# Kernel tuning notes

Measured on AMD Instinct MI355X. Metric: run time of the kernel, lower is better.

## Reference

```python
import jax, jax.numpy as jnp
import numpy as np

DIM = 768
NUM_HEADS = 12
HEAD_DIM = DIM // NUM_HEADS
SCALE = HEAD_DIM ** -0.5


def setup_inputs() -> dict:
    key = jax.random.key(0)
    k1, k2, k3, k4 = jax.random.split(key, 4)
    B, H, W = 8, 32, 32
    x = jax.random.normal(k1, (B, H, W, DIM), dtype=jnp.float32)
    s = DIM ** -0.5
    w_qkv = jax.random.normal(k2, (DIM, 3 * DIM), dtype=jnp.float32) * s
    w_proj = jax.random.normal(k3, (DIM, DIM), dtype=jnp.float32) * s
    b_proj = jax.random.normal(k4, (DIM,), dtype=jnp.float32) * 0.01
    return {"x": x, "w_qkv": w_qkv, "w_proj": w_proj, "b_proj": b_proj}


def reference(x, w_qkv, w_proj, b_proj):
    B, H, W, C = x.shape
    N = H * W
    qkv = (x.reshape(B, N, C) @ w_qkv).reshape(B, N, 3, NUM_HEADS, HEAD_DIM)
    q, k, v = jnp.moveaxis(qkv, 2, 0)  # each (B, N, h, d)
    # scores: (B, h, N, N)
    attn = jnp.einsum('bnhd,bmhd->bhnm', q * SCALE, k)
    attn = jax.nn.softmax(attn, axis=-1)
    out = jnp.einsum('bhnm,bmhd->bnhd', attn, v).reshape(B, H, W, C)
    return out @ w_proj + b_proj
```

## Files before the change

kernel.cpp:

```cpp
#include <hip/hip_runtime.h>

typedef _Float16 half_t;
typedef __attribute__((ext_vector_type(4))) _Float16 half4;
typedef __attribute__((ext_vector_type(8))) _Float16 half8;
typedef __attribute__((ext_vector_type(4))) float floatx4;

#define MFMA_F16(A,B,C)  __builtin_amdgcn_mfma_f32_16x16x32_f16(A,B,C,0,0,0)

typedef __attribute__((address_space(1))) const void gvoid_t;
typedef __attribute__((address_space(3))) void svoid_t;

__device__ __forceinline__ void async_copy16(const half_t* g, half_t* l) {
    __builtin_amdgcn_global_load_lds((gvoid_t*)g, (svoid_t*)l, 16, 0, 0);
}

__global__ __launch_bounds__(256)
void prep_kernel(const float* __restrict__ x, const float* __restrict__ w_qkv,
                 const float* __restrict__ w_proj, half_t* __restrict__ xh,
                 half_t* __restrict__ wqkvT, half_t* __restrict__ wprojT)
{
    __shared__ half_t tile[64 * 65];
    const int id = blockIdx.x, tid = threadIdx.x;
    if (id < 6144) {
        size_t e = (size_t)id * 1024 + tid * 4;
        float4 f = *(const float4*)(x + e);
        half4 h = { (half_t)f.x, (half_t)f.y, (half_t)f.z, (half_t)f.w };
        *(half4*)(xh + e) = h;
        return;
    }
    const float* src; half_t* dst; int lds, tr0, tc0;
    if (id < 6576) { int t = id - 6144; src = w_qkv; dst = wqkvT; lds = 2304;
                     tr0 = (t / 36) * 64; tc0 = (t % 36) * 64; }
    else           { int t = id - 6576; src = w_proj; dst = wprojT; lds = 768;
                     tr0 = (t / 12) * 64; tc0 = (t % 12) * 64; }
    #pragma unroll
    for (int i = 0; i < 4; i++) {
        int e = tid + i * 256, r = e >> 4, c4 = (e & 15) << 2;
        float4 f = *(const float4*)(src + (size_t)(tr0 + r) * lds + tc0 + c4);
        tile[(c4 + 0) * 65 + r] = (half_t)f.x;
        tile[(c4 + 1) * 65 + r] = (half_t)f.y;
        tile[(c4 + 2) * 65 + r] = (half_t)f.z;
        tile[(c4 + 3) * 65 + r] = (half_t)f.w;
    }
    __syncthreads();
    #pragma unroll
    for (int i = 0; i < 4; i++) {
        int e = tid + i * 256, c = e >> 4, r4 = (e & 15) << 2;
        half4 h = { tile[c * 65 + r4], tile[c * 65 + r4 + 1],
                    tile[c * 65 + r4 + 2], tile[c * 65 + r4 + 3] };
        *(half4*)(dst + (size_t)(tc0 + c) * 768 + tr0 + r4) = h;
    }
}

__global__ __launch_bounds__(256, 3)
void gemm_qkv(const half_t* __restrict__ A, const half_t* __restrict__ Bt,
              half_t* __restrict__ q_ws, half_t* __restrict__ k_ws,
              half_t* __restrict__ v_ws)
{
    __shared__ half_t As[2][128 * 32];
    __shared__ half_t Bs[2][192 * 32];

    const int lin  = blockIdx.x;
    const int xcd  = lin & 7, rest = lin >> 3;
    const int m0 = ((rest / 12) * 8 + xcd) * 128;
    const int n0 = (rest % 12) * 192;

    const int tid  = threadIdx.x;
    const int lane = tid & 63;
    const int w    = tid >> 6;
    const int wm   = w >> 1, wn = w & 1;
    const int quad = lane >> 4, l16 = lane & 15;

    const int b0p = (lane ^ (lane >> 2) ^ (lane >> 4)) & 1;
    const int b1p = ((lane >> 1) ^ (lane >> 3)) & 1;
    const int b2p = ((lane >> 2) ^ (lane >> 4)) & 1;
    const int row_log = ((lane >> 2) & 0xC) | ((lane >> 2) & 2) | b2p;
    const int q_log   = (b1p << 1) | b0p;

    const int foff = ((((l16 << 2) | quad) ^ (l16 & 7)) << 3);

    const half_t* a_src0 = A  + (size_t)(m0 + (w*2+0)*16 + row_log) * 768 + q_log*8;
    const half_t* a_src1 = A  + (size_t)(m0 + (w*2+1)*16 + row_log) * 768 + q_log*8;
    const half_t* b_src0 = Bt + (size_t)(n0 + (w*3+0)*16 + row_log) * 768 + q_log*8;
    const half_t* b_src1 = Bt + (size_t)(n0 + (w*3+1)*16 + row_log) * 768 + q_log*8;
    const half_t* b_src2 = Bt + (size_t)(n0 + (w*3+2)*16 + row_log) * 768 + q_log*8;

    floatx4 acc[4][6];
    #pragma unroll
    for (int i = 0; i < 4; i++)
        #pragma unroll
        for (int j = 0; j < 6; j++) acc[i][j] = (floatx4)0.0f;

    async_copy16(a_src0, &As[0][(w*2+0)*512]);
    async_copy16(a_src1, &As[0][(w*2+1)*512]);
    async_copy16(b_src0, &Bs[0][(w*3+0)*512]);
    async_copy16(b_src1, &Bs[0][(w*3+1)*512]);
    async_copy16(b_src2, &Bs[0][(w*3+2)*512]);
    __syncthreads();

    for (int t = 0; t < 24; ++t) {
        const int cur = t & 1;
        if (t < 23) {
            const int ko = (t + 1) * 32;
            async_copy16(a_src0 + ko, &As[cur ^ 1][(w*2+0)*512]);
            async_copy16(a_src1 + ko, &As[cur ^ 1][(w*2+1)*512]);
            async_copy16(b_src0 + ko, &Bs[cur ^ 1][(w*3+0)*512]);
            async_copy16(b_src1 + ko, &Bs[cur ^ 1][(w*3+1)*512]);
            async_copy16(b_src2 + ko, &Bs[cur ^ 1][(w*3+2)*512]);
        }
        half8 a[4], b[6];
        #pragma unroll
        for (int mi = 0; mi < 4; mi++)
            a[mi] = *(const half8*)(&As[cur][(wm*4 + mi) * 512 + foff]);
        #pragma unroll
        for (int ni = 0; ni < 6; ni++)
            b[ni] = *(const half8*)(&Bs[cur][(wn*6 + ni) * 512 + foff]);
        #pragma unroll
        for (int mi = 0; mi < 4; mi++)
            #pragma unroll
            for (int ni = 0; ni < 6; ni++)
                acc[mi][ni] = MFMA_F16(a[mi], b[ni], acc[mi][ni]);
        __syncthreads();
    }

    const int sel  = (n0 >= 1536) ? 2 : (n0 >= 768 ? 1 : 0);
    const int rem0 = n0 - sel * 768;
    const int bb   = m0 >> 10;
    const int t0   = m0 & 1023;
    const int rw   = wm * 64;

    if (sel == 0) {
        #pragma unroll
        for (int mi = 0; mi < 4; mi++)
            #pragma unroll
            for (int ni = 0; ni < 6; ni++) {
                int cb = rem0 + wn*96 + ni*16;
                int hh = cb >> 6;
                int d  = (cb & 63) + l16;
                size_t base = (size_t)(bb * 12 + hh) * 65536;
                int tok = t0 + rw + mi*16 + quad*4;
                half4 hv = { (half_t)(acc[mi][ni][0] * 0.125f),
                             (half_t)(acc[mi][ni][1] * 0.125f),
                             (half_t)(acc[mi][ni][2] * 0.125f),
                             (half_t)(acc[mi][ni][3] * 0.125f) };
                *(half4*)(q_ws + base + (size_t)d * 1024 + tok) = hv;
            }
    } else if (sel == 1) {
        #pragma unroll
        for (int mi = 0; mi < 4; mi++)
            #pragma unroll
            for (int ni = 0; ni < 6; ni++) {
                int cb = rem0 + wn*96 + ni*16;
                int hh = cb >> 6;
                int d  = (cb & 63) + l16;
                size_t base = (size_t)(bb * 12 + hh) * 65536;
                #pragma unroll
                for (int r = 0; r < 4; r++) {
                    int tok = t0 + rw + mi*16 + quad*4 + r;
                    k_ws[base + (size_t)tok * 64 + d] = (half_t)acc[mi][ni][r];
                }
            }
    } else {
        #pragma unroll
        for (int mi = 0; mi < 4; mi++)
            #pragma unroll
            for (int ni = 0; ni < 6; ni++) {
                int cb = rem0 + wn*96 + ni*16;
                int hh = cb >> 6;
                int d  = (cb & 63) + l16;
                size_t base = (size_t)(bb * 12 + hh) * 65536;
                int tokb = t0 + rw + (mi >> 1) * 32;
                int tokp = tokb | (quad << 3) | ((mi & 1) << 2);
                half4 hv = { (half_t)acc[mi][ni][0], (half_t)acc[mi][ni][1],
                             (half_t)acc[mi][ni][2], (half_t)acc[mi][ni][3] };
                *(half4*)(v_ws + base + (size_t)d * 1024 + tokp) = hv;
            }
    }
}

__global__ __launch_bounds__(256, 2)
void gemm_proj(const half_t* __restrict__ A, const half_t* __restrict__ Bt,
               float* __restrict__ Cout, const float* __restrict__ bias)
{
    __shared__ half_t As[128 * 64];
    __shared__ half_t Bs[128 * 64];

    const int lin  = blockIdx.x;
    const int xcd  = lin & 7, rest = lin >> 3;
    const int m0 = ((rest / 6) * 8 + xcd) * 128;
    const int n0 = (rest % 6) * 128;

    const int tid  = threadIdx.x;
    const int lane = tid & 63;
    const int w    = tid >> 6;
    const int wm   = w >> 1, wn = w & 1;
    const int quad = lane >> 4, l16 = lane & 15;
    const int lrow = lane >> 3;
    const int lcc  = (lane & 7) ^ lrow;
    const int xsw  = l16 & 7;

    const half_t* Ag = A  + (size_t)(m0 + w * 32 + lrow) * 768 + lcc * 8;
    const half_t* Bg = Bt + (size_t)(n0 + w * 32 + lrow) * 768 + lcc * 8;

    floatx4 acc[4][4];
    #pragma unroll
    for (int i = 0; i < 4; i++)
        #pragma unroll
        for (int j = 0; j < 4; j++) acc[i][j] = (floatx4)0.0f;

    for (int k0 = 0; k0 < 768; k0 += 64) {
        #pragma unroll
        for (int i = 0; i < 4; i++) {
            async_copy16(Ag + (size_t)(i * 8) * 768 + k0, As + (w * 4 + i) * 512);
            async_copy16(Bg + (size_t)(i * 8) * 768 + k0, Bs + (w * 4 + i) * 512);
        }
        __syncthreads();

        #pragma unroll
        for (int ks = 0; ks < 2; ks++) {
            const int co = (((ks << 2) + quad) ^ xsw) * 8;
            half8 a[4], b[4];
            #pragma unroll
            for (int mi = 0; mi < 4; mi++)
                a[mi] = *(const half8*)(As + (wm * 64 + mi * 16 + l16) * 64 + co);
            #pragma unroll
            for (int ni = 0; ni < 4; ni++)
                b[ni] = *(const half8*)(Bs + (wn * 64 + ni * 16 + l16) * 64 + co);
            #pragma unroll
            for (int mi = 0; mi < 4; mi++)
                #pragma unroll
                for (int ni = 0; ni < 4; ni++)
                    acc[mi][ni] = MFMA_F16(a[mi], b[ni], acc[mi][ni]);
        }
        __syncthreads();
    }

    float bias_v[4];
    #pragma unroll
    for (int ni = 0; ni < 4; ni++)
        bias_v[ni] = bias[n0 + wn * 64 + ni * 16 + l16];
    float* scratch = (w < 2 ? (float*)As : (float*)Bs) + (w & 1) * 1152;
    #pragma unroll
    for (int mi = 0; mi < 4; mi++) {
        #pragma unroll
        for (int ni = 0; ni < 4; ni++)
            #pragma unroll
            for (int r = 0; r < 4; r++)
                scratch[(quad * 4 + r) * 72 + ni * 16 + l16] =
                    acc[mi][ni][r] + bias_v[ni];
        #pragma unroll
        for (int i = 0; i < 4; i++) {
            int f = quad + i * 4;
            float4 v4 = *(const float4*)(scratch + l16 * 72 + f * 4);
            int gm = m0 + wm * 64 + mi * 16 + l16;
            *(float4*)(Cout + (size_t)gm * 768 + n0 + wn * 64 + f * 4) = v4;
        }
    }
}

__global__ __launch_bounds__(256, 3)
void attn_kernel(const half_t* __restrict__ qT, const half_t* __restrict__ k,
                 const half_t* __restrict__ vT, half_t* __restrict__ a_ws)
{
    __shared__ __align__(16) half_t Kb[2][4096];
    __shared__ __align__(16) half_t Vb[2][4096];
    __shared__ __align__(16) half_t Qs[64 * 128];

    const int lin  = blockIdx.x;
    const int xcd  = lin & 7, rest = lin >> 3;
    const int qc   = rest & 7;
    const int bh   = (rest >> 3) * 8 + xcd;

    const int tid  = threadIdx.x;
    const int lane = tid & 63;
    const int w    = tid >> 6;
    const int quad = lane >> 4, l16 = lane & 15;

    const half_t* qg = qT + (size_t)bh * 65536;
    const half_t* kg = k  + (size_t)bh * 65536;
    const half_t* vg = vT + (size_t)bh * 65536;

    const int srow = lane >> 3;
    const int sch  = (lane & 7) ^ srow;

    #pragma unroll
    for (int j = 0; j < 4; j++) {
        int d0 = w * 16 + j * 4;
        async_copy16(qg + (size_t)(d0 + (lane >> 4)) * 1024 + qc * 128 + (lane & 15) * 8,
                     &Qs[d0 * 128]);
    }
    #pragma unroll
    for (int j = 0; j < 2; j++) {
        int row = j * 32 + w * 8;
        async_copy16(kg + (size_t)(row + srow) * 64 + sch * 8, &Kb[0][row * 64]);
        async_copy16(vg + (size_t)(row + srow) * 1024 + sch * 8, &Vb[0][row * 64]);
    }
    __syncthreads();

    half8 qf[2][2];
    #pragma unroll
    for (int T = 0; T < 2; T++)
        #pragma unroll
        for (int ks = 0; ks < 2; ks++)
            #pragma unroll
            for (int j = 0; j < 8; j++)
                qf[T][ks][j] = Qs[(ks * 32 + quad * 8 + j) * 128
                                  + T * 64 + w * 16 + l16];

    floatx4 acc_o[2][4];
    floatx4 lacc[2];
    #pragma unroll
    for (int T = 0; T < 2; T++) {
        lacc[T] = (floatx4)0.0f;
        #pragma unroll
        for (int dt = 0; dt < 4; dt++) acc_o[T][dt] = (floatx4)0.0f;
    }

    const int xsw = l16 & 7;
    const half8 vone = { (half_t)1.0f, (half_t)1.0f, (half_t)1.0f, (half_t)1.0f,
                         (half_t)1.0f, (half_t)1.0f, (half_t)1.0f, (half_t)1.0f };

    for (int kt = 0; kt < 16; kt++) {
        const int cb = kt & 1;
        __syncthreads();
        if (kt < 15) {
            #pragma unroll
            for (int j = 0; j < 2; j++) {
                int row = j * 32 + w * 8;
                async_copy16(kg + (size_t)((kt + 1) * 64 + row + srow) * 64 + sch * 8,
                             &Kb[cb ^ 1][row * 64]);
                async_copy16(vg + (size_t)(row + srow) * 1024 + (kt + 1) * 64 + sch * 8,
                             &Vb[cb ^ 1][row * 64]);
            }
        }
        const half_t* Kc = Kb[cb];
        const half_t* Vc = Vb[cb];

        floatx4 sc[2][4];
        #pragma unroll
        for (int T = 0; T < 2; T++)
            #pragma unroll
            for (int mt = 0; mt < 4; mt++) sc[T][mt] = (floatx4)0.0f;
        #pragma unroll
        for (int ks = 0; ks < 2; ks++)
            #pragma unroll
            for (int mt = 0; mt < 4; mt++) {
                half8 kf = *(const half8*)(Kc + (mt * 16 + l16) * 64
                                              + (((ks << 2) + quad) ^ xsw) * 8);
                sc[0][mt] = MFMA_F16(kf, qf[0][ks], sc[0][mt]);
                sc[1][mt] = MFMA_F16(kf, qf[1][ks], sc[1][mt]);
            }

        half8 pa[2][2];
        #pragma unroll
        for (int T = 0; T < 2; T++)
            #pragma unroll
            for (int g = 0; g < 2; g++) {
                half8 ph;
                #pragma unroll
                for (int r = 0; r < 4; r++) ph[r]     = (half_t)__expf(sc[T][2 * g][r]);
                #pragma unroll
                for (int r = 0; r < 4; r++) ph[4 + r] = (half_t)__expf(sc[T][2 * g + 1][r]);
                pa[T][g] = ph;
            }

        #pragma unroll
        for (int g = 0; g < 2; g++) {
            lacc[0] = MFMA_F16(pa[0][g], vone, lacc[0]);
            lacc[1] = MFMA_F16(pa[1][g], vone, lacc[1]);
            #pragma unroll
            for (int dt = 0; dt < 4; dt++) {
                half8 vb = *(const half8*)(Vc + (dt * 16 + l16) * 64
                                              + ((((g << 2) + quad) ^ xsw) << 3));
                acc_o[0][dt] = MFMA_F16(pa[0][g], vb, acc_o[0][dt]);
                acc_o[1][dt] = MFMA_F16(pa[1][g], vb, acc_o[1][dt]);
            }
        }
    }

    const int b = bh / 12, h = bh - (bh / 12) * 12;
    #pragma unroll
    for (int T = 0; T < 2; T++)
        #pragma unroll
        for (int r = 0; r < 4; r++) {
            float inv = 1.0f / lacc[T][r];
            int n = qc * 128 + T * 64 + w * 16 + quad * 4 + r;
            half_t* op = a_ws + ((size_t)(b * 1024 + n)) * 768 + h * 64;
            #pragma unroll
            for (int dt = 0; dt < 4; dt++)
                op[dt * 16 + l16] = (half_t)(acc_o[T][dt][r] * inv);
        }
}

extern "C" void kernel_launch(void* const* d_in, const int* in_sizes, int n_in,
                              void* d_out, int out_size, void* d_ws, size_t ws_size,
                              hipStream_t stream)
{
    (void)in_sizes; (void)n_in; (void)out_size; (void)ws_size;
    const float* x      = (const float*)d_in[0];
    const float* w_qkv  = (const float*)d_in[1];
    const float* w_proj = (const float*)d_in[2];
    const float* b_proj = (const float*)d_in[3];
    float* out = (float*)d_out;

    half_t* ws     = (half_t*)d_ws;
    half_t* q_ws   = ws;
    half_t* k_ws   = ws + 6291456;
    half_t* v_ws   = ws + 2 * 6291456;
    half_t* xh     = ws + 3 * 6291456;
    half_t* wqkvT  = ws + 4 * 6291456;
    half_t* wprojT = wqkvT + 1769472;
    half_t* a_ws   = xh;

    prep_kernel<<<dim3(6720), dim3(256), 0, stream>>>(x, w_qkv, w_proj, xh, wqkvT, wprojT);
    gemm_qkv<<<dim3(768), dim3(256), 0, stream>>>(xh, wqkvT, q_ws, k_ws, v_ws);
    attn_kernel<<<dim3(768), dim3(256), 0, stream>>>(q_ws, k_ws, v_ws, a_ws);
    gemm_proj<<<dim3(384), dim3(256), 0, stream>>>(a_ws, wprojT, out, b_proj);
}
```

Measured before the change: 178.4 us.

## Deepen QKV GEMM pipeline to four LDS stages with prefetch distance two

Moves the QKV projection GEMM from double buffering to a 4-slot LDS ring with loads issued two tiles ahead. Each iteration waits on explicit vmcnt counts plus a raw s_barrier instead of a full __syncthreads, so global-to-LDS loads for later tiles stay in flight. MFMA issue priority is raised during the compute phase. The larger LDS footprint drops the occupancy target from 3 to 2 blocks per CU. The hand-counted vmcnt values assume exactly five loads per stage.

```diff
diff --git a/kernel.cpp b/kernel.cpp
--- a/kernel.cpp
+++ b/kernel.cpp
@@ -52,13 +52,13 @@
     }
 }
 
-__global__ __launch_bounds__(256, 3)
+__global__ __launch_bounds__(256, 2)
 void gemm_qkv(const half_t* __restrict__ A, const half_t* __restrict__ Bt,
               half_t* __restrict__ q_ws, half_t* __restrict__ k_ws,
               half_t* __restrict__ v_ws)
 {
-    __shared__ half_t As[2][128 * 32];
-    __shared__ half_t Bs[2][192 * 32];
+    __shared__ half_t As[4][128 * 32];
+    __shared__ half_t Bs[4][192 * 32];
 
     const int lin  = blockIdx.x;
     const int xcd  = lin & 7, rest = lin >> 3;
@@ -91,23 +91,27 @@
         #pragma unroll
         for (int j = 0; j < 6; j++) acc[i][j] = (floatx4)0.0f;
 
-    async_copy16(a_src0, &As[0][(w*2+0)*512]);
-    async_copy16(a_src1, &As[0][(w*2+1)*512]);
-    async_copy16(b_src0, &Bs[0][(w*3+0)*512]);
-    async_copy16(b_src1, &Bs[0][(w*3+1)*512]);
-    async_copy16(b_src2, &Bs[0][(w*3+2)*512]);
-    __syncthreads();
-
+    #define STAGE(BUF, KO)                                            \
+        do {                                                          \
+            async_copy16(a_src0 + (KO), &As[BUF][(w*2+0)*512]);       \
+            async_copy16(a_src1 + (KO), &As[BUF][(w*2+1)*512]);       \
+            async_copy16(b_src0 + (KO), &Bs[BUF][(w*3+0)*512]);       \
+            async_copy16(b_src1 + (KO), &Bs[BUF][(w*3+1)*512]);       \
+            async_copy16(b_src2 + (KO), &Bs[BUF][(w*3+2)*512]);       \
+        } while (0)
+
+    STAGE(0, 0);
+    STAGE(1, 32);
+
+    #pragma unroll 1
     for (int t = 0; t < 24; ++t) {
-        const int cur = t & 1;
-        if (t < 23) {
-            const int ko = (t + 1) * 32;
-            async_copy16(a_src0 + ko, &As[cur ^ 1][(w*2+0)*512]);
-            async_copy16(a_src1 + ko, &As[cur ^ 1][(w*2+1)*512]);
-            async_copy16(b_src0 + ko, &Bs[cur ^ 1][(w*3+0)*512]);
-            async_copy16(b_src1 + ko, &Bs[cur ^ 1][(w*3+1)*512]);
-            async_copy16(b_src2 + ko, &Bs[cur ^ 1][(w*3+2)*512]);
-        }
+        const int cur = t & 3;
+        if (t < 22) STAGE((t + 2) & 3, (t + 2) * 32);
+        if (t < 22)       asm volatile("s_waitcnt vmcnt(10)" ::: "memory");
+        else if (t == 22) asm volatile("s_waitcnt vmcnt(5)"  ::: "memory");
+        else              asm volatile("s_waitcnt vmcnt(0)"  ::: "memory");
+        __builtin_amdgcn_s_barrier();
+
         half8 a[4], b[6];
         #pragma unroll
         for (int mi = 0; mi < 4; mi++)
@@ -115,13 +119,16 @@
         #pragma unroll
         for (int ni = 0; ni < 6; ni++)
             b[ni] = *(const half8*)(&Bs[cur][(wn*6 + ni) * 512 + foff]);
+
+        __builtin_amdgcn_s_setprio(1);
         #pragma unroll
         for (int mi = 0; mi < 4; mi++)
             #pragma unroll
             for (int ni = 0; ni < 6; ni++)
                 acc[mi][ni] = MFMA_F16(a[mi], b[ni], acc[mi][ni]);
-        __syncthreads();
-    }
+        __builtin_amdgcn_s_setprio(0);
+    }
+    #undef STAGE
 
     const int sel  = (n0 >= 1536) ? 2 : (n0 >= 768 ? 1 : 0);
     const int rem0 = n0 - sel * 768;
```

After: 181.5 us. About the same (+1.7%).
